# Kernel optimization log

Measured on AMD Instinct MI355X. Metric: run time of the kernel, lower is better.

## Reference

```python
import jax, jax.numpy as jnp
import numpy as np

N = 100000       # nodes
E = 1600000      # edges (before self-loops)
IN = 128         # input feature dim
HID = 16         # per-head hidden dim (layer 1)
HEADS = 8        # heads (layer 1)
OUT = 64         # output classes (layer 2, heads=1)
NEG_SLOPE = 0.2  # PyG GATConv default leaky relu slope


def setup_inputs() -> dict:
    key = jax.random.key(0)
    ks = jax.random.split(key, 10)
    s = 0.05
    return {
        "x": jax.random.normal(ks[0], (N, IN), jnp.float32),
        "edge_index": jax.random.randint(ks[1], (2, E), 0, N, dtype=jnp.int64),
        "W1": jax.random.normal(ks[2], (IN, HEADS * HID), jnp.float32) * s,
        "att_src1": jax.random.normal(ks[3], (HEADS, HID), jnp.float32) * s,
        "att_dst1": jax.random.normal(ks[4], (HEADS, HID), jnp.float32) * s,
        "bias1": jnp.zeros((HEADS * HID,), jnp.float32),
        "W2": jax.random.normal(ks[5], (HEADS * HID, OUT), jnp.float32) * s,
        "att_src2": jax.random.normal(ks[6], (1, OUT), jnp.float32) * s,
        "att_dst2": jax.random.normal(ks[7], (1, OUT), jnp.float32) * s,
        "bias2": jnp.zeros((OUT,), jnp.float32),
    }


def gat_conv(x, edge_index, W, att_src, att_dst, bias, heads, ch):
    """PyG GATConv: linear -> per-edge LeakyReLU score -> segment softmax over
    incoming edges -> scatter-sum aggregation. Self-loops added (PyG default)."""
    n = x.shape[0]
    loop = jnp.arange(n, dtype=edge_index.dtype)
    src = jnp.concatenate([edge_index[0], loop])  # [E2]
    dst = jnp.concatenate([edge_index[1], loop])  # [E2]

    h = (x @ W).reshape(n, heads, ch)                       # [N,H,C]
    a_src = jnp.einsum('nhc,hc->nh', h, att_src)            # [N,H]
    a_dst = jnp.einsum('nhc,hc->nh', h, att_dst)            # [N,H]

    e = a_src[src] + a_dst[dst]                             # [E2,H]
    e = jnp.where(e > 0, e, NEG_SLOPE * e)                  # leaky relu

    # numerically stable segment softmax over edges grouped by dst
    m = jax.ops.segment_max(e, dst, num_segments=n)         # [N,H]
    p = jnp.exp(e - m[dst])                                 # [E2,H]
    denom = jax.ops.segment_sum(p, dst, num_segments=n)     # [N,H]
    alpha = p / (denom[dst] + 1e-16)                        # [E2,H]

    out = jax.ops.segment_sum(h[src] * alpha[:, :, None], dst, num_segments=n)
    return out.reshape(n, heads * ch) + bias                # concat heads


def reference(x, edge_index, W1, att_src1, att_dst1, bias1, W2, att_src2, att_dst2, bias2):
    h = jax.nn.relu(gat_conv(x, edge_index, W1, att_src1, att_dst1, bias1, HEADS, HID))
    # dropout is identity in eval mode
    out = gat_conv(h, edge_index, W2, att_src2, att_dst2, bias2, 1, OUT)
    return jax.nn.log_softmax(out, axis=1)
```

## Files before the change

kernel.cpp:

```cpp
#include <hip/hip_runtime.h>
#include <hip/hip_bf16.h>

#define N_NODES 100000
#define N_EDGES 1600000
#define NEG_SLOPE 0.2f

#define BUCK_SHIFT 7
#define NBUCK ((N_NODES + 127) >> BUCK_SHIFT)
#define B1 256
#define CHUNK ((N_EDGES + B1 - 1) / B1)

#define SCAN_ITEMS 4
#define SCAN_BLK 256
#define SCAN_CHUNK (SCAN_BLK * SCAN_ITEMS)
#define NSCAN (NBUCK * B1)
#define SCAN_NB ((NSCAN + SCAN_CHUNK - 1) / SCAN_CHUNK)

typedef _Float16 f16;
typedef _Float16 f16x8 __attribute__((ext_vector_type(8)));
typedef _Float16 f16x2 __attribute__((ext_vector_type(2)));
typedef float f32x4 __attribute__((ext_vector_type(4)));
typedef float f32x2v __attribute__((ext_vector_type(2)));

__device__ __forceinline__ bool edges_are_i64(const void* p) {
    const unsigned long long* q = (const unsigned long long*)p;
    bool ok = true;
#pragma unroll
    for (int i = 0; i < 8; i++)
        if (q[i] >= (unsigned long long)N_NODES) ok = false;
    return ok;
}
__device__ __forceinline__ int edge_src(const void* ei, int j, bool i64) {
    return i64 ? (int)((const long long*)ei)[j] : ((const int*)ei)[j];
}
__device__ __forceinline__ int edge_dst(const void* ei, int j, bool i64) {
    return i64 ? (int)((const long long*)ei)[N_EDGES + j] : ((const int*)ei)[N_EDGES + j];
}

__global__ __launch_bounds__(256) void bhist_k(const void* __restrict__ ei,
                                               int* __restrict__ bh) {
    __shared__ int hist[NBUCK];
    bool i64 = edges_are_i64(ei);
    int bl = blockIdx.x, t = threadIdx.x;
    for (int i = t; i < NBUCK; i += 256) hist[i] = 0;
    __syncthreads();
    int lo = bl * CHUNK, hi = min(lo + CHUNK, N_EDGES);
    for (int j = lo + t; j < hi; j += 256)
        atomicAdd(&hist[edge_dst(ei, j, i64) >> BUCK_SHIFT], 1);
    __syncthreads();
    for (int i = t; i < NBUCK; i += 256) bh[i * B1 + bl] = hist[i];
}

__global__ __launch_bounds__(SCAN_BLK) void scan1_k(const int* __restrict__ in,
                                                    int* __restrict__ outp,
                                                    int* __restrict__ bsum, int n) {
    __shared__ int lds[SCAN_BLK];
    int t = threadIdx.x, b = blockIdx.x;
    int base = b * SCAN_CHUNK + t * SCAN_ITEMS;
    int v[SCAN_ITEMS];
    int s = 0;
#pragma unroll
    for (int i = 0; i < SCAN_ITEMS; i++) {
        v[i] = (base + i < n) ? in[base + i] : 0;
        s += v[i];
    }
    lds[t] = s;
    __syncthreads();
    for (int o = 1; o < SCAN_BLK; o <<= 1) {
        int x = (t >= o) ? lds[t - o] : 0;
        __syncthreads();
        lds[t] += x;
        __syncthreads();
    }
    if (t == SCAN_BLK - 1) bsum[b] = lds[t];
    int run = lds[t] - s;
#pragma unroll
    for (int i = 0; i < SCAN_ITEMS; i++) {
        if (base + i < n) outp[base + i] = run;
        run += v[i];
    }
}

__global__ __launch_bounds__(256) void scan2_k(int* __restrict__ bsum, int nb) {
    __shared__ int lds[256];
    int t = threadIdx.x;
    int v = (t < nb) ? bsum[t] : 0;
    lds[t] = v;
    __syncthreads();
    for (int o = 1; o < 256; o <<= 1) {
        int x = (t >= o) ? lds[t - o] : 0;
        __syncthreads();
        lds[t] += x;
        __syncthreads();
    }
    if (t < nb) bsum[t] = lds[t] - v;
}

__global__ void scan3_k(int* __restrict__ outp, const int* __restrict__ bsum, int n) {
    int i = blockIdx.x * blockDim.x + threadIdx.x;
    if (i < n) outp[i] += bsum[i / SCAN_CHUNK];
}

__global__ __launch_bounds__(256) void bscatter_k(const void* __restrict__ ei,
                                                  const int* __restrict__ s,
                                                  int2* __restrict__ be) {
    __shared__ int cur[NBUCK];
    bool i64 = edges_are_i64(ei);
    int bl = blockIdx.x, t = threadIdx.x;
    for (int i = t; i < NBUCK; i += 256) cur[i] = s[i * B1 + bl];
    __syncthreads();
    int lo = bl * CHUNK, hi = min(lo + CHUNK, N_EDGES);
    for (int j = lo + t; j < hi; j += 256) {
        int d = edge_dst(ei, j, i64);
        int sr = edge_src(ei, j, i64);
        int pos = atomicAdd(&cur[d >> BUCK_SHIFT], 1);
        be[pos] = make_int2(d, sr);
    }
}

__global__ __launch_bounds__(256) void bcsr_k(const int* __restrict__ s,
                                              const int2* __restrict__ be,
                                              int* __restrict__ rp,
                                              int* __restrict__ csrc) {
    __shared__ int cnt[128];
    __shared__ int pre[128];
    int b = blockIdx.x, t = threadIdx.x;
    int beg = s[b * B1];
    int end = (b == NBUCK - 1) ? N_EDGES : s[(b + 1) * B1];
    if (t < 128) cnt[t] = 0;
    __syncthreads();
    for (int j = beg + t; j < end; j += 256)
        atomicAdd(&cnt[be[j].x & 127], 1);
    __syncthreads();
    if (t < 128) pre[t] = cnt[t];
    __syncthreads();
    for (int o = 1; o < 128; o <<= 1) {
        int x = 0;
        if (t < 128 && t >= o) x = pre[t - o];
        __syncthreads();
        if (t < 128) pre[t] += x;
        __syncthreads();
    }
    if (t < 128) {
        int node = (b << BUCK_SHIFT) + t;
        int excl = pre[t] - cnt[t];
        if (node < N_NODES) rp[node] = beg + excl;
        cnt[t] = excl;
    }
    if (b == 0 && t == 0) rp[N_NODES] = N_EDGES;
    __syncthreads();
    for (int j = beg + t; j < end; j += 256) {
        int2 e = be[j];
        int pos = beg + atomicAdd(&cnt[e.x & 127], 1);
        csrc[pos] = e.y;
    }
}

template <int NCT>
__global__ void cvt_wfrag_k(const float* __restrict__ W, f16* __restrict__ wf) {
    int idx = blockIdx.x * blockDim.x + threadIdx.x;
    if (idx >= 4 * NCT * 512) return;
    int j = idx & 7;
    int lane = (idx >> 3) & 63;
    int ct = (idx >> 9) % NCT;
    int ks = (idx >> 9) / NCT;
    int k = ks * 32 + 8 * (lane >> 4) + j;
    int col = ct * 16 + (lane & 15);
    wf[idx] = (f16)W[k * (NCT * 16) + col];
}

template <int NCT, typename AT>
__global__ __launch_bounds__(256) void gemm_mfma(const AT* __restrict__ A,
                                                 const f16* __restrict__ wf,
                                                 f16* __restrict__ H, int n) {
    int lane = threadIdx.x & 63;
    int row0 = blockIdx.x * 64 + (threadIdx.x >> 6) * 16;
    int m = lane & 15, g = lane >> 4;
    f32x4 acc[NCT];
#pragma unroll
    for (int ct = 0; ct < NCT; ct++) acc[ct] = (f32x4){0.f, 0.f, 0.f, 0.f};

    int ar = row0 + m;
    if (ar >= n) ar = 0;
    const AT* arow = A + (size_t)ar * 128 + g * 8;
    const f16x8* bp = (const f16x8*)wf;
#pragma unroll
    for (int ks = 0; ks < 4; ks++) {
        f16x8 af;
        if constexpr (sizeof(AT) == 4) {
            const float4* p = (const float4*)(arow + ks * 32);
            float4 a = p[0], b = p[1];
            af[0] = (f16)a.x; af[1] = (f16)a.y; af[2] = (f16)a.z; af[3] = (f16)a.w;
            af[4] = (f16)b.x; af[5] = (f16)b.y; af[6] = (f16)b.z; af[7] = (f16)b.w;
        } else {
            af = *(const f16x8*)(arow + ks * 32);
        }
#pragma unroll
        for (int ct = 0; ct < NCT; ct++) {
            f16x8 bf = bp[(ks * NCT + ct) * 64 + lane];
            acc[ct] = __builtin_amdgcn_mfma_f32_16x16x32_f16(af, bf, acc[ct], 0, 0, 0);
        }
    }
#pragma unroll
    for (int ct = 0; ct < NCT; ct++)
#pragma unroll
        for (int r = 0; r < 4; r++) {
            int orow = row0 + g * 4 + r;
            if (orow < n) H[(size_t)orow * (NCT * 16) + ct * 16 + m] = (f16)acc[ct][r];
        }
}

template <int HEADS, int CH>
__global__ void att_scores(const f16* __restrict__ H, const float* __restrict__ att_s,
                           const float* __restrict__ att_d, float* __restrict__ a_s,
                           float* __restrict__ a_d, unsigned char* __restrict__ h8,
                           int n) {
    int idx = blockIdx.x * blockDim.x + threadIdx.x;
    if (idx >= n * HEADS) return;
    int node = idx / HEADS;
    int h = idx - node * HEADS;
    const f16x8* hp = (const f16x8*)(H + (size_t)node * (HEADS * CH) + h * CH);
    float vals[CH];
    float s = 0.f, d = 0.f;
#pragma unroll
    for (int c8 = 0; c8 < CH / 8; c8++) {
        f16x8 v = hp[c8];
#pragma unroll
        for (int j = 0; j < 8; j++) {
            float x = (float)v[j];
            vals[c8 * 8 + j] = x;
            s = fmaf(x, att_s[h * CH + c8 * 8 + j], s);
            d = fmaf(x, att_d[h * CH + c8 * 8 + j], d);
        }
    }
    a_s[idx] = s;
    a_d[idx] = d;

    int4* dst = (int4*)(h8 + (size_t)node * (HEADS * CH) + h * CH);
#pragma unroll
    for (int t = 0; t < CH / 16; t++) {
        int w[4];
#pragma unroll
        for (int q = 0; q < 4; q++) {
            int u = __builtin_amdgcn_cvt_pk_fp8_f32(vals[t * 16 + 4 * q],
                                                    vals[t * 16 + 4 * q + 1], 0, false);
            u = __builtin_amdgcn_cvt_pk_fp8_f32(vals[t * 16 + 4 * q + 2],
                                                vals[t * 16 + 4 * q + 3], u, true);
            w[q] = u;
        }
        dst[t] = make_int4(w[0], w[1], w[2], w[3]);
    }
}

__global__ __launch_bounds__(256) void aggr1_k(const int* __restrict__ rp,
                                               const int* __restrict__ csrc,
                                               const float* __restrict__ a_s,
                                               const float* __restrict__ a_d,
                                               const unsigned char* __restrict__ h8,
                                               const float* __restrict__ bias,
                                               f16* __restrict__ out) {
    int lane = threadIdx.x & 63;
    int d = blockIdx.x * 4 + (threadIdx.x >> 6);
    if (d >= N_NODES) return;
    int head = lane >> 3;
    int shead = lane & 7;

    float ed_v = a_d[d * 8 + head];
    float ed_s = a_d[d * 8 + shead];

    float e0 = a_s[d * 8 + head] + ed_v;
    e0 = e0 > 0.f ? e0 : NEG_SLOPE * e0;
    float w0 = __expf(e0);
    unsigned short u0 = *(const unsigned short*)(h8 + (size_t)d * 128 + 2 * lane);
    f32x2v v0 = __builtin_amdgcn_cvt_pk_f32_fp8((int)u0, false);
    float den = w0, nx = w0 * v0[0], ny = w0 * v0[1];

    int beg = rp[d], end = rp[d + 1];
    for (int cbeg = beg; cbeg < end; cbeg += 8) {
        int e = cbeg + (lane >> 3);
        int s = 0;
        float w = 0.f;
        if (e < end) {
            s = csrc[e];
            float es = a_s[s * 8 + shead] + ed_s;
            es = es > 0.f ? es : NEG_SLOPE * es;
            w = __expf(es);
        }
#pragma unroll
        for (int k = 0; k < 8; k++) {
            float we = __shfl(w, k * 8 + head, 64);
            int se = __shfl(s, k * 8, 64);
            unsigned short uu = *(const unsigned short*)(h8 + (size_t)se * 128 + 2 * lane);
            f32x2v v = __builtin_amdgcn_cvt_pk_f32_fp8((int)uu, false);
            den += we;
            nx = fmaf(we, v[0], nx);
            ny = fmaf(we, v[1], ny);
        }
    }
    float inv = 1.f / (den + 1e-16f);
    float2 b = ((const float2*)bias)[lane];
    f16x2 r;
    r[0] = (f16)fmaxf(fmaf(nx, inv, b.x), 0.f);
    r[1] = (f16)fmaxf(fmaf(ny, inv, b.y), 0.f);
    ((f16x2*)out)[(size_t)d * 64 + lane] = r;
}

__global__ __launch_bounds__(256) void aggr2_k(const int* __restrict__ rp,
                                               const int* __restrict__ csrc,
                                               const float* __restrict__ a_s,
                                               const float* __restrict__ a_d,
                                               const unsigned char* __restrict__ h8,
                                               const float* __restrict__ bias,
                                               float* __restrict__ out) {
    int lane = threadIdx.x & 63;
    int d = blockIdx.x * 4 + (threadIdx.x >> 6);
    if (d >= N_NODES) return;

    float ed = a_d[d];
    float e0 = a_s[d] + ed;
    e0 = e0 > 0.f ? e0 : NEG_SLOPE * e0;
    float w0 = __expf(e0);
    float v0 = __builtin_amdgcn_cvt_f32_fp8((int)h8[(size_t)d * 64 + lane], 0);
    float den = w0, num = w0 * v0;

    int beg = rp[d], end = rp[d + 1];
    for (int cbeg = beg; cbeg < end; cbeg += 8) {
        int e = cbeg + (lane & 7);
        int s = 0;
        float w = 0.f;
        if (e < end) {
            s = csrc[e];
            float es = a_s[s] + ed;
            es = es > 0.f ? es : NEG_SLOPE * es;
            w = __expf(es);
        }
#pragma unroll
        for (int k = 0; k < 8; k++) {
            float we = __shfl(w, k, 64);
            int se = __shfl(s, k, 64);
            float v = __builtin_amdgcn_cvt_f32_fp8((int)h8[(size_t)se * 64 + lane], 0);
            den += we;
            num = fmaf(we, v, num);
        }
    }
    float z = num / (den + 1e-16f) + bias[lane];

    float m = z;
#pragma unroll
    for (int o = 32; o > 0; o >>= 1) m = fmaxf(m, __shfl_xor(m, o, 64));
    float p = __expf(z - m);
    float ssum = p;
#pragma unroll
    for (int o = 32; o > 0; o >>= 1) ssum += __shfl_xor(ssum, o, 64);
    out[(size_t)d * 64 + lane] = z - m - logf(ssum);
}

extern "C" void kernel_launch(void* const* d_in, const int* in_sizes, int n_in,
                              void* d_out, int out_size, void* d_ws, size_t ws_size,
                              hipStream_t stream) {
    const float* x   = (const float*)d_in[0];
    const void*  ei  = d_in[1];
    const float* W1  = (const float*)d_in[2];
    const float* as1 = (const float*)d_in[3];
    const float* ad1 = (const float*)d_in[4];
    const float* b1  = (const float*)d_in[5];
    const float* W2  = (const float*)d_in[6];
    const float* as2 = (const float*)d_in[7];
    const float* ad2 = (const float*)d_in[8];
    const float* b2  = (const float*)d_in[9];
    float* out = (float*)d_out;

    f16*   h1   = (f16*)d_ws;
    f16*   out1 = h1 + (size_t)N_NODES * 128;
    unsigned char* h8 = (unsigned char*)(out1 + (size_t)N_NODES * 128);
    f16*   w1f  = (f16*)(h8 + (size_t)N_NODES * 128);
    f16*   w2f  = w1f + 16384;
    float* a_s  = (float*)(w2f + 8192);
    float* a_d  = a_s + (size_t)N_NODES * 8;
    int*   rp   = (int*)(a_d + (size_t)N_NODES * 8);
    int*   bh   = rp + (N_NODES + 64);
    int*   bsum = bh + NSCAN;
    int*   csrc = bsum + 256;
    int2*  be   = (int2*)(csrc + N_EDGES);
    f16*   h2   = h1;

    bhist_k<<<B1, 256, 0, stream>>>(ei, bh);
    scan1_k<<<SCAN_NB, SCAN_BLK, 0, stream>>>(bh, bh, bsum, NSCAN);
    scan2_k<<<1, 256, 0, stream>>>(bsum, SCAN_NB);
    scan3_k<<<(NSCAN + 255) / 256, 256, 0, stream>>>(bh, bsum, NSCAN);
    bscatter_k<<<B1, 256, 0, stream>>>(ei, bh, be);
    bcsr_k<<<NBUCK, 256, 0, stream>>>(bh, be, rp, csrc);

    cvt_wfrag_k<8><<<(4 * 8 * 512 + 255) / 256, 256, 0, stream>>>(W1, w1f);
    cvt_wfrag_k<4><<<(4 * 4 * 512 + 255) / 256, 256, 0, stream>>>(W2, w2f);

    gemm_mfma<8, float><<<(N_NODES + 63) / 64, 256, 0, stream>>>(x, w1f, h1, N_NODES);
    att_scores<8, 16><<<(N_NODES * 8 + 255) / 256, 256, 0, stream>>>(h1, as1, ad1, a_s, a_d, h8, N_NODES);
    aggr1_k<<<(N_NODES + 3) / 4, 256, 0, stream>>>(rp, csrc, a_s, a_d, h8, b1, out1);

    gemm_mfma<4, f16><<<(N_NODES + 63) / 64, 256, 0, stream>>>(out1, w2f, h2, N_NODES);
    att_scores<1, 64><<<(N_NODES + 255) / 256, 256, 0, stream>>>(h2, as2, ad2, a_s, a_d, h8, N_NODES);
    aggr2_k<<<(N_NODES + 3) / 4, 256, 0, stream>>>(rp, csrc, a_s, a_d, h8, b2, out);
}
```

Before: 229.4 us.

## Aggregate 8 edges in parallel per wavefront and pack bucket entries into one int

The aggregation kernels now give each group of 8 lanes its own edge. Each lane loads a 16-byte (layer 1) or 8-byte (layer 2) fp8 feature slice, accumulates in registers, and the groups are combined with a cross-lane xor reduction at the end. This replaces the serial per-edge shuffle loop in which every lane loaded only 1-2 bytes per edge, so gathers get wider and more edges are in flight. The bucket scatter also packs src and the low dst bits into a single int, halving that intermediate's traffic. In exchange there are more registers and a final shuffle reduction, and the layer-2 log-softmax is reorganized per lane group.

```diff
diff --git a/kernel.cpp b/kernel.cpp
--- a/kernel.cpp
+++ b/kernel.cpp
@@ -35,6 +35,15 @@
 }
 __device__ __forceinline__ int edge_dst(const void* ei, int j, bool i64) {
     return i64 ? (int)((const long long*)ei)[N_EDGES + j] : ((const int*)ei)[N_EDGES + j];
+}
+
+__device__ __forceinline__ void acc4(f32x4& a, float w, int u) {
+    f32x2v p0 = __builtin_amdgcn_cvt_pk_f32_fp8(u, false);
+    f32x2v p1 = __builtin_amdgcn_cvt_pk_f32_fp8(u, true);
+    a[0] = fmaf(w, p0[0], a[0]);
+    a[1] = fmaf(w, p0[1], a[1]);
+    a[2] = fmaf(w, p1[0], a[2]);
+    a[3] = fmaf(w, p1[1], a[3]);
 }
 
 __global__ __launch_bounds__(256) void bhist_k(const void* __restrict__ ei,
@@ -103,7 +112,7 @@
 
 __global__ __launch_bounds__(256) void bscatter_k(const void* __restrict__ ei,
                                                   const int* __restrict__ s,
-                                                  int2* __restrict__ be) {
+                                                  int* __restrict__ be) {
     __shared__ int cur[NBUCK];
     bool i64 = edges_are_i64(ei);
     int bl = blockIdx.x, t = threadIdx.x;
@@ -114,12 +123,12 @@
         int d = edge_dst(ei, j, i64);
         int sr = edge_src(ei, j, i64);
         int pos = atomicAdd(&cur[d >> BUCK_SHIFT], 1);
-        be[pos] = make_int2(d, sr);
+        be[pos] = (sr << BUCK_SHIFT) | (d & 127);
     }
 }
 
 __global__ __launch_bounds__(256) void bcsr_k(const int* __restrict__ s,
-                                              const int2* __restrict__ be,
+                                              const int* __restrict__ be,
                                               int* __restrict__ rp,
                                               int* __restrict__ csrc) {
     __shared__ int cnt[128];
@@ -130,7 +139,7 @@
     if (t < 128) cnt[t] = 0;
     __syncthreads();
     for (int j = beg + t; j < end; j += 256)
-        atomicAdd(&cnt[be[j].x & 127], 1);
+        atomicAdd(&cnt[be[j] & 127], 1);
     __syncthreads();
     if (t < 128) pre[t] = cnt[t];
     __syncthreads();
@@ -150,9 +159,9 @@
     if (b == 0 && t == 0) rp[N_NODES] = N_EDGES;
     __syncthreads();
     for (int j = beg + t; j < end; j += 256) {
-        int2 e = be[j];
-        int pos = beg + atomicAdd(&cnt[e.x & 127], 1);
-        csrc[pos] = e.y;
+        int e = be[j];
+        int pos = beg + atomicAdd(&cnt[e & 127], 1);
+        csrc[pos] = e >> BUCK_SHIFT;
     }
 }
 
@@ -262,47 +271,61 @@
     int lane = threadIdx.x & 63;
     int d = blockIdx.x * 4 + (threadIdx.x >> 6);
     if (d >= N_NODES) return;
-    int head = lane >> 3;
-    int shead = lane & 7;
-
-    float ed_v = a_d[d * 8 + head];
-    float ed_s = a_d[d * 8 + shead];
-
-    float e0 = a_s[d * 8 + head] + ed_v;
-    e0 = e0 > 0.f ? e0 : NEG_SLOPE * e0;
-    float w0 = __expf(e0);
-    unsigned short u0 = *(const unsigned short*)(h8 + (size_t)d * 128 + 2 * lane);
-    f32x2v v0 = __builtin_amdgcn_cvt_pk_f32_fp8((int)u0, false);
-    float den = w0, nx = w0 * v0[0], ny = w0 * v0[1];
+    int j = lane >> 3;
+    int c = lane & 7;
+
+    float ed = a_d[d * 8 + c];
+    f32x4 acc0 = {0.f, 0.f, 0.f, 0.f}, acc1 = {0.f, 0.f, 0.f, 0.f};
+    f32x4 acc2 = {0.f, 0.f, 0.f, 0.f}, acc3 = {0.f, 0.f, 0.f, 0.f};
+    float den = 0.f;
+
+    if (j == 0) {
+        float e0 = a_s[d * 8 + c] + ed;
+        e0 = e0 > 0.f ? e0 : NEG_SLOPE * e0;
+        float w0 = __expf(e0);
+        den = w0;
+        int4 u = *(const int4*)(h8 + (size_t)d * 128 + 16 * c);
+        acc4(acc0, w0, u.x); acc4(acc1, w0, u.y);
+        acc4(acc2, w0, u.z); acc4(acc3, w0, u.w);
+    }
 
     int beg = rp[d], end = rp[d + 1];
     for (int cbeg = beg; cbeg < end; cbeg += 8) {
-        int e = cbeg + (lane >> 3);
-        int s = 0;
-        float w = 0.f;
-        if (e < end) {
-            s = csrc[e];
-            float es = a_s[s * 8 + shead] + ed_s;
-            es = es > 0.f ? es : NEG_SLOPE * es;
-            w = __expf(es);
-        }
-#pragma unroll
-        for (int k = 0; k < 8; k++) {
-            float we = __shfl(w, k * 8 + head, 64);
-            int se = __shfl(s, k * 8, 64);
-            unsigned short uu = *(const unsigned short*)(h8 + (size_t)se * 128 + 2 * lane);
-            f32x2v v = __builtin_amdgcn_cvt_pk_f32_fp8((int)uu, false);
-            den += we;
-            nx = fmaf(we, v[0], nx);
-            ny = fmaf(we, v[1], ny);
+        int e = cbeg + j;
+        int ee = e < end ? e : end - 1;
+        int s = csrc[ee];
+        float es = a_s[s * 8 + c] + ed;
+        es = es > 0.f ? es : NEG_SLOPE * es;
+        float w = (e < end) ? __expf(es) : 0.f;
+        den += w;
+        int4 u = *(const int4*)(h8 + (size_t)s * 128 + 16 * c);
+        acc4(acc0, w, u.x); acc4(acc1, w, u.y);
+        acc4(acc2, w, u.z); acc4(acc3, w, u.w);
+    }
+
+#pragma unroll
+    for (int o = 8; o < 64; o <<= 1) {
+        den += __shfl_xor(den, o, 64);
+#pragma unroll
+        for (int i = 0; i < 4; i++) {
+            acc0[i] += __shfl_xor(acc0[i], o, 64);
+            acc1[i] += __shfl_xor(acc1[i], o, 64);
+            acc2[i] += __shfl_xor(acc2[i], o, 64);
+            acc3[i] += __shfl_xor(acc3[i], o, 64);
         }
     }
     float inv = 1.f / (den + 1e-16f);
-    float2 b = ((const float2*)bias)[lane];
+
+    f32x4 tA = (j & 2) ? acc1 : acc0;
+    f32x4 tB = (j & 2) ? acc3 : acc2;
+    f32x4 t  = (j & 4) ? tB : tA;
+    float vx = (j & 1) ? t[2] : t[0];
+    float vy = (j & 1) ? t[3] : t[1];
+    float2 b = ((const float2*)bias)[8 * c + j];
     f16x2 r;
-    r[0] = (f16)fmaxf(fmaf(nx, inv, b.x), 0.f);
-    r[1] = (f16)fmaxf(fmaf(ny, inv, b.y), 0.f);
-    ((f16x2*)out)[(size_t)d * 64 + lane] = r;
+    r[0] = (f16)fmaxf(fmaf(vx, inv, b.x), 0.f);
+    r[1] = (f16)fmaxf(fmaf(vy, inv, b.y), 0.f);
+    ((f16x2*)out)[(size_t)d * 64 + 8 * c + j] = r;
 }
 
 __global__ __launch_bounds__(256) void aggr2_k(const int* __restrict__ rp,
@@ -315,44 +338,73 @@
     int lane = threadIdx.x & 63;
     int d = blockIdx.x * 4 + (threadIdx.x >> 6);
     if (d >= N_NODES) return;
+    int j = lane >> 3;
+    int q = lane & 7;
 
     float ed = a_d[d];
-    float e0 = a_s[d] + ed;
-    e0 = e0 > 0.f ? e0 : NEG_SLOPE * e0;
-    float w0 = __expf(e0);
-    float v0 = __builtin_amdgcn_cvt_f32_fp8((int)h8[(size_t)d * 64 + lane], 0);
-    float den = w0, num = w0 * v0;
+    f32x4 accA = {0.f, 0.f, 0.f, 0.f}, accB = {0.f, 0.f, 0.f, 0.f};
+    float den = 0.f;
+
+    if (j == 0) {
+        float e0 = a_s[d] + ed;
+        e0 = e0 > 0.f ? e0 : NEG_SLOPE * e0;
+        float w0 = __expf(e0);
+        den = w0;
+        int2 u = *(const int2*)(h8 + (size_t)d * 64 + 8 * q);
+        acc4(accA, w0, u.x); acc4(accB, w0, u.y);
+    }
 
     int beg = rp[d], end = rp[d + 1];
     for (int cbeg = beg; cbeg < end; cbeg += 8) {
-        int e = cbeg + (lane & 7);
-        int s = 0;
-        float w = 0.f;
-        if (e < end) {
-            s = csrc[e];
-            float es = a_s[s] + ed;
-            es = es > 0.f ? es : NEG_SLOPE * es;
-            w = __expf(es);
-        }
-#pragma unroll
-        for (int k = 0; k < 8; k++) {
-            float we = __shfl(w, k, 64);
-            int se = __shfl(s, k, 64);
-            float v = __builtin_amdgcn_cvt_f32_fp8((int)h8[(size_t)se * 64 + lane], 0);
-            den += we;
-            num = fmaf(we, v, num);
-        }
-    }
-    float z = num / (den + 1e-16f) + bias[lane];
-
-    float m = z;
-#pragma unroll
-    for (int o = 32; o > 0; o >>= 1) m = fmaxf(m, __shfl_xor(m, o, 64));
-    float p = __expf(z - m);
-    float ssum = p;
-#pragma unroll
-    for (int o = 32; o > 0; o >>= 1) ssum += __shfl_xor(ssum, o, 64);
-    out[(size_t)d * 64 + lane] = z - m - logf(ssum);
+        int e = cbeg + j;
+        int ee = e < end ? e : end - 1;
+        int s = csrc[ee];
+        float es = a_s[s] + ed;
+        es = es > 0.f ? es : NEG_SLOPE * es;
+        float w = (e < end) ? __expf(es) : 0.f;
+        den += w;
+        int2 u = *(const int2*)(h8 + (size_t)s * 64 + 8 * q);
+        acc4(accA, w, u.x); acc4(accB, w, u.y);
+    }
+
+#pragma unroll
+    for (int o = 8; o < 64; o <<= 1) {
+        den += __shfl_xor(den, o, 64);
+#pragma unroll
+        for (int i = 0; i < 4; i++) {
+            accA[i] += __shfl_xor(accA[i], o, 64);
+            accB[i] += __shfl_xor(accB[i], o, 64);
+        }
+    }
+    float inv = 1.f / (den + 1e-16f);
+
+    const float4* bp = (const float4*)bias;
+    float4 b0 = bp[2 * q], b1 = bp[2 * q + 1];
+    float z[8];
+    z[0] = fmaf(accA[0], inv, b0.x); z[1] = fmaf(accA[1], inv, b0.y);
+    z[2] = fmaf(accA[2], inv, b0.z); z[3] = fmaf(accA[3], inv, b0.w);
+    z[4] = fmaf(accB[0], inv, b1.x); z[5] = fmaf(accB[1], inv, b1.y);
+    z[6] = fmaf(accB[2], inv, b1.z); z[7] = fmaf(accB[3], inv, b1.w);
+
+    float m = z[0];
+#pragma unroll
+    for (int i = 1; i < 8; i++) m = fmaxf(m, z[i]);
+#pragma unroll
+    for (int o = 1; o < 8; o <<= 1) m = fmaxf(m, __shfl_xor(m, o, 64));
+    float p = 0.f;
+#pragma unroll
+    for (int i = 0; i < 8; i++) p += __expf(z[i] - m);
+#pragma unroll
+    for (int o = 1; o < 8; o <<= 1) p += __shfl_xor(p, o, 64);
+    float lse = m + logf(p);
+
+    if (j == 0) {
+        float4 o0 = {z[0] - lse, z[1] - lse, z[2] - lse, z[3] - lse};
+        float4 o1 = {z[4] - lse, z[5] - lse, z[6] - lse, z[7] - lse};
+        float4* op = (float4*)(out + (size_t)d * 64 + 8 * q);
+        op[0] = o0;
+        op[1] = o1;
+    }
 }
 
 extern "C" void kernel_launch(void* const* d_in, const int* in_sizes, int n_in,
@@ -381,7 +433,7 @@
     int*   bh   = rp + (N_NODES + 64);
     int*   bsum = bh + NSCAN;
     int*   csrc = bsum + 256;
-    int2*  be   = (int2*)(csrc + N_EDGES);
+    int*   be   = csrc + N_EDGES;
     f16*   h2   = h1;
 
     bhist_k<<<B1, 256, 0, stream>>>(ei, bh);
```

New measurement: 232.3 us, median of 4. About the same (+1.3%).
